# Kernel tuning notes

Hardware: AMD Instinct MI355X
Metric: run time of the kernel (lower is better)

## Reference

```python
import jax, jax.numpy as jnp
import numpy as np

D_MODEL = 1024
N_HEADS = 16
HEAD_DIM = D_MODEL // N_HEADS


def setup_inputs() -> dict:
    key = jax.random.key(0)
    ks = jax.random.split(key, 11)
    B, S = 4, 2048
    scale = 1.0 / np.sqrt(D_MODEL)
    inp = {
        "Q": jax.random.normal(ks[0], (B, S, D_MODEL), jnp.float32),
        "K": jax.random.normal(ks[1], (B, S, D_MODEL), jnp.float32),
        "V": jax.random.normal(ks[2], (B, S, D_MODEL), jnp.float32),
        "Wq": jax.random.normal(ks[3], (D_MODEL, D_MODEL), jnp.float32) * scale,
        "bq": jnp.zeros((D_MODEL,), jnp.float32),
        "Wk": jax.random.normal(ks[4], (D_MODEL, D_MODEL), jnp.float32) * scale,
        "bk": jnp.zeros((D_MODEL,), jnp.float32),
        "Wv": jax.random.normal(ks[5], (D_MODEL, D_MODEL), jnp.float32) * scale,
        "bv": jnp.zeros((D_MODEL,), jnp.float32),
        "Wo": jax.random.normal(ks[6], (D_MODEL, D_MODEL), jnp.float32) * scale,
        "bo": jnp.zeros((D_MODEL,), jnp.float32),
    }
    return inp


def reference(Q, K, V, Wq, bq, Wk, bk, Wv, bv, Wo, bo):
    B, S, _ = Q.shape
    # Linear projections (torch nn.Linear: x @ W.T + b)
    q = Q @ Wq.T + bq
    k = K @ Wk.T + bk
    v = V @ Wv.T + bv
    # [B, S, H, Dh] -> [B, H, S, Dh]
    q = q.reshape(B, S, N_HEADS, HEAD_DIM).transpose(0, 2, 1, 3)
    k = k.reshape(B, S, N_HEADS, HEAD_DIM).transpose(0, 2, 1, 3)
    v = v.reshape(B, S, N_HEADS, HEAD_DIM).transpose(0, 2, 1, 3)
    inv_sqrt_dh = 1.0 / np.sqrt(HEAD_DIM)
    scores = jnp.einsum("bhqd,bhkd->bhqk", q, k) * inv_sqrt_dh  # [B,H,S,S]
    attn = jax.nn.softmax(scores, axis=-1)
    out = jnp.einsum("bhqk,bhkd->bhqd", attn, v)  # [B,H,S,Dh]
    out = out.transpose(0, 2, 1, 3).reshape(B, S, D_MODEL)
    return out @ Wo.T + bo
```

## Files before the change

### kernel.cpp

```cpp
#include <hip/hip_runtime.h>
#include <hip/hip_bf16.h>
#include <stdint.h>
#include <stddef.h>


typedef __bf16 bf16_t;
typedef __bf16 bf16x4 __attribute__((ext_vector_type(4)));
typedef __bf16 bf16x8 __attribute__((ext_vector_type(8)));
typedef float f32x4 __attribute__((ext_vector_type(4)));

#define D_MODEL 1024
#define M_ROWS  8192
#define S_LEN   2048
#define N_HEADS 16
#define HEAD_DIM 64
#define GBK 32
#define NT (D_MODEL / GBK)

__device__ __forceinline__ void async_copy16(void* lds, const void* g) {
    __builtin_amdgcn_global_load_lds(
        (const __attribute__((address_space(1))) void*)g,
        (__attribute__((address_space(3))) void*)lds, 16, 0, 0);
}

__device__ __forceinline__ uint32_t cvt_pk_bf16(float lo, float hi) {
    uint32_t r;
    asm("v_cvt_pk_bf16_f32 %0, %1, %2" : "=v"(r) : "v"(lo), "v"(hi));
    return r;
}

__global__ __launch_bounds__(256) void conv_w(
    const float* __restrict__ s0, const float* __restrict__ s1, const float* __restrict__ s2,
    bf16_t* __restrict__ d0, bf16_t* __restrict__ d1, bf16_t* __restrict__ d2)
{
    const float* s; bf16_t* d;
    if (blockIdx.y == 0)      { s = s0; d = d0; }
    else if (blockIdx.y == 1) { s = s1; d = d1; }
    else                      { s = s2; d = d2; }
    const int i = (blockIdx.x * 256 + threadIdx.x) * 8;
    const f32x4 a = *(const f32x4*)(s + i);
    const f32x4 b = *(const f32x4*)(s + i + 4);
    bf16x8 o;
#pragma unroll
    for (int j = 0; j < 4; j++) { o[j] = (bf16_t)a[j]; o[4 + j] = (bf16_t)b[j]; }
    *(bf16x8*)(d + i) = o;
}

__global__ __launch_bounds__(256, 3) void gemm_proj(
    const float* __restrict__ A0, const bf16_t* __restrict__ W0, const float* __restrict__ b0,
    const float* __restrict__ A1, const bf16_t* __restrict__ W1, const float* __restrict__ b1,
    const float* __restrict__ A2, const bf16_t* __restrict__ W2, const float* __restrict__ b2,
    bf16_t* C0, bf16_t* C1, bf16_t* C2)
{
    const int lin = blockIdx.x + ((int)blockIdx.y << 3) + ((int)blockIdx.z << 9);
    const int nl  = (lin & 7) * 192 + (lin >> 3);
    const int z   = nl >> 9;
    const int rem = nl & 511;
    const int bm0 = (rem >> 3) * 128;
    const int bn0 = (rem & 7) * 128;

    const float* A; const bf16_t* W; const float* bias; bf16_t* C;
    if (z == 0)      { A = A0; W = W0; bias = b0; C = C0; }
    else if (z == 1) { A = A1; W = W1; bias = b1; C = C1; }
    else             { A = A2; W = W2; bias = b2; C = C2; }
    const float cs = (z == 0) ? 0.125f : (z == 1) ? 1.4426950408889634f : 1.0f;

    __align__(16) __shared__ bf16_t sA[2][128 * 36];
    __align__(16) __shared__ bf16_t sW[2][128 * GBK];

    const int t    = threadIdx.x;
    const int lane = t & 63;
    const int w    = t >> 6;
    const int wm   = (w & 1) * 64;
    const int wn   = (w >> 1) * 64;
    const int q4   = lane >> 4;
    const int l16  = lane & 15;

    const int srow  = t >> 1;
    const int cbase = (t & 1) * 2;
    const float* aptr = &A[(size_t)(bm0 + srow) * D_MODEL + cbase * 8];

    auto stageW = [&](int buf, int kt) {
#pragma unroll
        for (int i = 0; i < 2; i++) {
            const int cid = i * 256 + t;
            const int row = cid >> 2;
            const int cg  = (cid & 3) ^ (row & 3);
            async_copy16(&sW[buf][cid * 8],
                         &W[(size_t)(bn0 + row) * D_MODEL + kt * GBK + cg * 8]);
        }
    };

    f32x4 arA[4], arB[4];
#pragma unroll
    for (int c = 0; c < 4; c++) {
        arA[c] = *(const f32x4*)(aptr + c * 4);
        arB[c] = *(const f32x4*)(aptr + GBK + c * 4);
    }
    stageW(0, 0);

    f32x4 acc[4][4];
    const f32x4 zero4 = {0.f, 0.f, 0.f, 0.f};
#pragma unroll
    for (int i = 0; i < 4; i++)
#pragma unroll
        for (int j = 0; j < 4; j++) acc[i][j] = zero4;

    auto body = [&](int kt, int buf, f32x4 (&ar)[4]) {
        bf16x8 abf[2];
#pragma unroll
        for (int c = 0; c < 4; c++)
#pragma unroll
            for (int j = 0; j < 4; j++)
                abf[c >> 1][(c & 1) * 4 + j] = (bf16_t)ar[c][j];
#pragma unroll
        for (int hb = 0; hb < 2; hb++) {
            const int slot = (cbase + hb) ^ (srow & 3);
            *(bf16x8*)&sA[buf][srow * 36 + slot * 8] = abf[hb];
        }
        __syncthreads();
        if (kt + 2 < NT) {
            const float* ap = aptr + (size_t)(kt + 2) * GBK;
#pragma unroll
            for (int c = 0; c < 4; c++) ar[c] = *(const f32x4*)(ap + c * 4);
        }
        if (kt + 1 < NT) stageW(buf ^ 1, kt + 1);

        bf16x8 af[4], bfr[4];
#pragma unroll
        for (int i = 0; i < 4; i++) {
            const int m = wm + i * 16 + l16;
            af[i]  = *(const bf16x8*)&sA[buf][m * 36 + (q4 ^ (m & 3)) * 8];
            const int n = wn + i * 16 + l16;
            bfr[i] = *(const bf16x8*)&sW[buf][n * GBK + (q4 ^ (n & 3)) * 8];
        }
#pragma unroll
        for (int i = 0; i < 4; i++)
#pragma unroll
            for (int j = 0; j < 4; j++)
                acc[i][j] = __builtin_amdgcn_mfma_f32_16x16x32_bf16(af[i], bfr[j], acc[i][j], 0, 0, 0);
    };

    for (int kt = 0; kt < NT; kt += 2) {
        body(kt,     0, arA);
        body(kt + 1, 1, arB);
    }

    if (z != 2) {
#pragma unroll
        for (int j = 0; j < 4; j++) {
            const int col = bn0 + wn + j * 16 + l16;
            const float bj = bias[col];
#pragma unroll
            for (int i = 0; i < 4; i++) {
                const int rowb = bm0 + wm + i * 16 + q4 * 4;
#pragma unroll
                for (int r = 0; r < 4; r++)
                    C[(size_t)(rowb + r) * D_MODEL + col] = (bf16_t)((acc[i][j][r] + bj) * cs);
            }
        }
    } else {
        const int bb = bm0 >> 11;
        const int sbase = (bm0 & 2047) + wm;
#pragma unroll
        for (int j = 0; j < 4; j++) {
            const int col = bn0 + wn + j * 16 + l16;
            const float bj = bias[col];
            bf16_t* ct = C + ((size_t)bb * 1024 + col) * 2048;
#pragma unroll
            for (int i = 0; i < 4; i++) {
                const int s0 = sbase + i * 16 + q4 * 4;
                const int s0p = (s0 & ~31) | (((s0 >> 2) & 3) << 3) | (((s0 >> 4) & 1) << 2);
                bf16x4 v4;
#pragma unroll
                for (int r = 0; r < 4; r++) v4[r] = (bf16_t)(acc[i][j][r] + bj);
                *(bf16x4*)&ct[s0p] = v4;
            }
        }
    }
}

__global__ __launch_bounds__(256, 3) void gemm_out(
    const bf16_t* __restrict__ A, const bf16_t* __restrict__ W,
    const float* __restrict__ bias, float* __restrict__ C)
{
    const int lin = blockIdx.x + ((int)blockIdx.y << 3);
    const int nl  = (lin & 7) * 64 + (lin >> 3);
    const int bm0 = (nl >> 3) * 128;
    const int bn0 = (nl & 7) * 128;

    __align__(16) __shared__ bf16_t sA[2][128 * GBK];
    __align__(16) __shared__ bf16_t sW[2][128 * GBK];

    const int t    = threadIdx.x;
    const int lane = t & 63;
    const int w    = t >> 6;
    const int wm   = (w & 1) * 64;
    const int wn   = (w >> 1) * 64;
    const int q4   = lane >> 4;
    const int l16  = lane & 15;

    auto stage = [&](int buf, int kt) {
#pragma unroll
        for (int i = 0; i < 2; i++) {
            const int cid = i * 256 + t;
            const int row = cid >> 2;
            const int cg  = (cid & 3) ^ (row & 3);
            async_copy16(&sA[buf][cid * 8],
                         &A[(size_t)(bm0 + row) * D_MODEL + kt * GBK + cg * 8]);
            async_copy16(&sW[buf][cid * 8],
                         &W[(size_t)(bn0 + row) * D_MODEL + kt * GBK + cg * 8]);
        }
    };

    stage(0, 0);

    f32x4 acc[4][4];
    const f32x4 zero4 = {0.f, 0.f, 0.f, 0.f};
#pragma unroll
    for (int i = 0; i < 4; i++)
#pragma unroll
        for (int j = 0; j < 4; j++) acc[i][j] = zero4;

    for (int kt = 0; kt < NT; ++kt) {
        const int buf = kt & 1;
        __syncthreads();
        if (kt + 1 < NT) stage(buf ^ 1, kt + 1);

        bf16x8 af[4], bfr[4];
#pragma unroll
        for (int i = 0; i < 4; i++) {
            const int m = wm + i * 16 + l16;
            af[i]  = *(const bf16x8*)&sA[buf][m * GBK + (q4 ^ (m & 3)) * 8];
            const int n = wn + i * 16 + l16;
            bfr[i] = *(const bf16x8*)&sW[buf][n * GBK + (q4 ^ (n & 3)) * 8];
        }
#pragma unroll
        for (int i = 0; i < 4; i++)
#pragma unroll
            for (int j = 0; j < 4; j++)
                acc[i][j] = __builtin_amdgcn_mfma_f32_16x16x32_bf16(af[i], bfr[j], acc[i][j], 0, 0, 0);
    }

#pragma unroll
    for (int j = 0; j < 4; j++) {
        const int col = bn0 + wn + j * 16 + l16;
        const float bj = bias[col];
#pragma unroll
        for (int i = 0; i < 4; i++) {
            const int rowb = bm0 + wm + i * 16 + q4 * 4;
#pragma unroll
            for (int r = 0; r < 4; r++)
                C[(size_t)(rowb + r) * D_MODEL + col] = acc[i][j][r] + bj;
        }
    }
}

#define KVT (S_LEN / 128)

__global__ __launch_bounds__(512, 3) void attn_fused(
    const bf16_t* __restrict__ q, const bf16_t* __restrict__ k,
    const bf16_t* __restrict__ vt, bf16_t* o)
{
    __align__(16) __shared__ bf16_t sK[2][128 * 64];
    __align__(16) __shared__ bf16_t sVt[2][64 * 128];

    const int t    = threadIdx.x;
    const int lane = t & 63;
    const int w    = t >> 6;
    const int head = blockIdx.x;
    const int b    = head >> 4;
    const int h    = head & 15;
    const size_t base = (size_t)b * S_LEN * D_MODEL + (size_t)h * HEAD_DIM;
    const bf16_t* vth = vt + ((size_t)b * 1024 + h * 64) * 2048;
    const int qt0  = blockIdx.y * 256;
    const int q4   = lane >> 4;
    const int l16  = lane & 15;

    bf16x8 qf[2][2];
#pragma unroll
    for (int mg = 0; mg < 2; mg++)
#pragma unroll
        for (int kk = 0; kk < 2; kk++)
            qf[mg][kk] = *(const bf16x8*)&q[base + (size_t)(qt0 + w * 32 + mg * 16 + l16) * D_MODEL + kk * 32 + q4 * 8];

    const f32x4 zero4 = {0.f, 0.f, 0.f, 0.f};
    f32x4 oacc[2][4];
#pragma unroll
    for (int mg = 0; mg < 2; mg++)
#pragma unroll
        for (int g = 0; g < 4; g++) oacc[mg][g] = zero4;
    f32x4 sacc[2] = {zero4, zero4};

    bf16x8 ones;
#pragma unroll
    for (int j = 0; j < 8; j++) ones[j] = (bf16_t)1.0f;

    auto stage = [&](int bf, int kt) {
        const int key0 = kt * 128;
#pragma unroll
        for (int i = 0; i < 2; i++) {
            const int cid = i * 512 + t;
            const int row = cid >> 3;
            const int cg  = (cid & 7) ^ (row & 7);
            async_copy16(&sK[bf][cid * 8], &k[base + (size_t)(key0 + row) * D_MODEL + cg * 8]);
        }
#pragma unroll
        for (int i = 0; i < 2; i++) {
            const int cid = i * 512 + t;
            const int dh  = cid >> 4;
            const int cg  = (cid & 15) ^ (dh & 15);
            async_copy16(&sVt[bf][cid * 8], &vth[(size_t)dh * 2048 + key0 + cg * 8]);
        }
    };

    stage(0, 0);
    asm volatile("s_waitcnt vmcnt(0)" ::: "memory");
    __builtin_amdgcn_s_barrier();
    __builtin_amdgcn_sched_barrier(0);

    for (int kt = 0; kt < KVT; ++kt) {
        const int cur = kt & 1;
        if (kt < KVT - 1) stage(cur ^ 1, kt + 1);

#pragma unroll
        for (int hh = 0; hh < 2; hh++) {
            f32x4 sc[2][4];
            __builtin_amdgcn_s_setprio(1);
#pragma unroll
            for (int ngl = 0; ngl < 4; ngl++) {
                const int key = (hh * 4 + ngl) * 16 + l16;
                const bf16x8 kf0 = *(const bf16x8*)&sK[cur][key * 64 + ((q4) ^ (key & 7)) * 8];
                const bf16x8 kf1 = *(const bf16x8*)&sK[cur][key * 64 + ((4 + q4) ^ (key & 7)) * 8];
#pragma unroll
                for (int mg = 0; mg < 2; mg++) {
                    sc[mg][ngl] = __builtin_amdgcn_mfma_f32_16x16x32_bf16(kf0, qf[mg][0], zero4, 0, 0, 0);
                    sc[mg][ngl] = __builtin_amdgcn_mfma_f32_16x16x32_bf16(kf1, qf[mg][1], sc[mg][ngl], 0, 0, 0);
                }
            }
            __builtin_amdgcn_s_setprio(0);

            bf16x8 pf[2][2];
#pragma unroll
            for (int mg = 0; mg < 2; mg++) {
#pragma unroll
                for (int ngl = 0; ngl < 4; ngl++)
#pragma unroll
                    for (int r = 0; r < 4; r++)
                        sc[mg][ngl][r] = exp2f(sc[mg][ngl][r]);
#pragma unroll
                for (int cl = 0; cl < 2; cl++) {
                    union { uint32_t u[4]; bf16x8 v; } pk;
#pragma unroll
                    for (int dw = 0; dw < 4; dw++) {
                        const int c = cl * 2 + (dw >> 1);
                        const int e = (dw & 1) * 2;
                        pk.u[dw] = cvt_pk_bf16(sc[mg][c][e], sc[mg][c][e + 1]);
                    }
                    pf[mg][cl] = pk.v;
                }
            }

            __builtin_amdgcn_s_setprio(1);
#pragma unroll
            for (int cl = 0; cl < 2; cl++) {
                const int cb = (hh * 2 + cl) * 4;
#pragma unroll
                for (int g = 0; g < 4; g++) {
                    const int dh = g * 16 + l16;
                    const bf16x8 vf = *(const bf16x8*)&sVt[cur][dh * 128 + ((cb + q4) ^ l16) * 8];
#pragma unroll
                    for (int mg = 0; mg < 2; mg++)
                        oacc[mg][g] = __builtin_amdgcn_mfma_f32_16x16x32_bf16(pf[mg][cl], vf, oacc[mg][g], 0, 0, 0);
                }
#pragma unroll
                for (int mg = 0; mg < 2; mg++)
                    sacc[mg] = __builtin_amdgcn_mfma_f32_16x16x32_bf16(pf[mg][cl], ones, sacc[mg], 0, 0, 0);
            }
            __builtin_amdgcn_s_setprio(0);
        }

        asm volatile("s_waitcnt vmcnt(0)" ::: "memory");
        __builtin_amdgcn_s_barrier();
        __builtin_amdgcn_sched_barrier(0);
    }

#pragma unroll
    for (int mg = 0; mg < 2; mg++)
#pragma unroll
        for (int r = 0; r < 4; r++) {
            const float inv = 1.0f / sacc[mg][r];
            const size_t rowoff = base + (size_t)(qt0 + w * 32 + mg * 16 + q4 * 4 + r) * D_MODEL;
#pragma unroll
            for (int g = 0; g < 4; g++)
                o[rowoff + g * 16 + l16] = (bf16_t)(oacc[mg][g][r] * inv);
        }
}

extern "C" void kernel_launch(void* const* d_in, const int* in_sizes, int n_in,
                              void* d_out, int out_size, void* d_ws, size_t ws_size,
                              hipStream_t stream) {
    const float* Q  = (const float*)d_in[0];
    const float* K  = (const float*)d_in[1];
    const float* V  = (const float*)d_in[2];
    const float* Wq = (const float*)d_in[3];
    const float* bq = (const float*)d_in[4];
    const float* Wk = (const float*)d_in[5];
    const float* bk = (const float*)d_in[6];
    const float* Wv = (const float*)d_in[7];
    const float* bv = (const float*)d_in[8];
    const float* Wo = (const float*)d_in[9];
    const float* bo = (const float*)d_in[10];
    float* out = (float*)d_out;

    bf16_t* qb  = (bf16_t*)d_ws;
    bf16_t* vb  = qb + (size_t)M_ROWS * D_MODEL;
    bf16_t* kb  = (bf16_t*)d_out;
    bf16_t* wqb = kb + (size_t)M_ROWS * D_MODEL;
    bf16_t* wkb = wqb + (size_t)D_MODEL * D_MODEL;
    bf16_t* wvb = wkb + (size_t)D_MODEL * D_MODEL;
    bf16_t* wob = vb;
    bf16_t* ob  = qb;

    conv_w<<<dim3(512, 3), dim3(256), 0, stream>>>(Wq, Wk, Wv, wqb, wkb, wvb);
    gemm_proj<<<dim3(8, 64, 3), dim3(256), 0, stream>>>(Q, wqb, bq, K, wkb, bk, V, wvb, bv, qb, kb, vb);
    attn_fused<<<dim3(4 * N_HEADS, S_LEN / 256), dim3(512), 0, stream>>>(qb, kb, vb, ob);
    conv_w<<<dim3(512, 1), dim3(256), 0, stream>>>(Wo, Wo, Wo, wob, wob, wob);
    gemm_out<<<dim3(8, 64), dim3(256), 0, stream>>>(ob, wob, bo, out);
}
```

Baseline: 375.9 us.

## Pipeline projection GEMM with one barrier per tile and adjust LDS swizzle

Result: faster. 358.3 us (-4.7%).

```diff
diff --git a/kernel.cpp b/kernel.cpp
--- a/kernel.cpp
+++ b/kernel.cpp
@@ -85,28 +85,12 @@
         for (int i = 0; i < 2; i++) {
             const int cid = i * 256 + t;
             const int row = cid >> 2;
-            const int cg  = (cid & 3) ^ (row & 3);
+            const int cg  = (cid & 3) ^ ((row >> 1) & 3);
             async_copy16(&sW[buf][cid * 8],
                          &W[(size_t)(bn0 + row) * D_MODEL + kt * GBK + cg * 8]);
         }
     };
-
-    f32x4 arA[4], arB[4];
-#pragma unroll
-    for (int c = 0; c < 4; c++) {
-        arA[c] = *(const f32x4*)(aptr + c * 4);
-        arB[c] = *(const f32x4*)(aptr + GBK + c * 4);
-    }
-    stageW(0, 0);
-
-    f32x4 acc[4][4];
-    const f32x4 zero4 = {0.f, 0.f, 0.f, 0.f};
-#pragma unroll
-    for (int i = 0; i < 4; i++)
-#pragma unroll
-        for (int j = 0; j < 4; j++) acc[i][j] = zero4;
-
-    auto body = [&](int kt, int buf, f32x4 (&ar)[4]) {
+    auto writeA = [&](int buf, f32x4 (&ar)[4]) {
         bf16x8 abf[2];
 #pragma unroll
         for (int c = 0; c < 4; c++)
@@ -118,13 +102,33 @@
             const int slot = (cbase + hb) ^ (srow & 3);
             *(bf16x8*)&sA[buf][srow * 36 + slot * 8] = abf[hb];
         }
-        __syncthreads();
+    };
+
+    stageW(0, 0);
+    f32x4 arA[4], arB[4];
+#pragma unroll
+    for (int c = 0; c < 4; c++) arA[c] = *(const f32x4*)(aptr + c * 4);
+#pragma unroll
+    for (int c = 0; c < 4; c++) arB[c] = *(const f32x4*)(aptr + GBK + c * 4);
+    writeA(0, arA);
+    asm volatile("s_waitcnt vmcnt(4) lgkmcnt(0)" ::: "memory");
+    __builtin_amdgcn_s_barrier();
+    __builtin_amdgcn_sched_barrier(0);
+
+    f32x4 acc[4][4];
+    const f32x4 zero4 = {0.f, 0.f, 0.f, 0.f};
+#pragma unroll
+    for (int i = 0; i < 4; i++)
+#pragma unroll
+        for (int j = 0; j < 4; j++) acc[i][j] = zero4;
+
+    auto body = [&](int kt, int buf, f32x4 (&arCur)[4], f32x4 (&arNext)[4]) {
+        if (kt + 1 < NT) stageW(buf ^ 1, kt + 1);
         if (kt + 2 < NT) {
             const float* ap = aptr + (size_t)(kt + 2) * GBK;
 #pragma unroll
-            for (int c = 0; c < 4; c++) ar[c] = *(const f32x4*)(ap + c * 4);
-        }
-        if (kt + 1 < NT) stageW(buf ^ 1, kt + 1);
+            for (int c = 0; c < 4; c++) arNext[c] = *(const f32x4*)(ap + c * 4);
+        }
 
         bf16x8 af[4], bfr[4];
 #pragma unroll
@@ -132,18 +136,25 @@
             const int m = wm + i * 16 + l16;
             af[i]  = *(const bf16x8*)&sA[buf][m * 36 + (q4 ^ (m & 3)) * 8];
             const int n = wn + i * 16 + l16;
-            bfr[i] = *(const bf16x8*)&sW[buf][n * GBK + (q4 ^ (n & 3)) * 8];
+            bfr[i] = *(const bf16x8*)&sW[buf][n * GBK + (q4 ^ ((n >> 1) & 3)) * 8];
         }
 #pragma unroll
         for (int i = 0; i < 4; i++)
 #pragma unroll
             for (int j = 0; j < 4; j++)
                 acc[i][j] = __builtin_amdgcn_mfma_f32_16x16x32_bf16(af[i], bfr[j], acc[i][j], 0, 0, 0);
+
+        __builtin_amdgcn_sched_barrier(0);
+        if (kt + 1 < NT) writeA(buf ^ 1, arCur);
+        if (kt + 2 < NT) asm volatile("s_waitcnt vmcnt(4) lgkmcnt(0)" ::: "memory");
+        else             asm volatile("s_waitcnt vmcnt(0) lgkmcnt(0)" ::: "memory");
+        __builtin_amdgcn_s_barrier();
+        __builtin_amdgcn_sched_barrier(0);
     };
 
     for (int kt = 0; kt < NT; kt += 2) {
-        body(kt,     0, arA);
-        body(kt + 1, 1, arB);
+        body(kt,     0, arB, arA);
+        body(kt + 1, 1, arA, arB);
     }
 
     if (z != 2) {
@@ -205,7 +216,7 @@
         for (int i = 0; i < 2; i++) {
             const int cid = i * 256 + t;
             const int row = cid >> 2;
-            const int cg  = (cid & 3) ^ (row & 3);
+            const int cg  = (cid & 3) ^ ((row >> 1) & 3);
             async_copy16(&sA[buf][cid * 8],
                          &A[(size_t)(bm0 + row) * D_MODEL + kt * GBK + cg * 8]);
             async_copy16(&sW[buf][cid * 8],
@@ -231,9 +242,9 @@
 #pragma unroll
         for (int i = 0; i < 4; i++) {
             const int m = wm + i * 16 + l16;
-            af[i]  = *(const bf16x8*)&sA[buf][m * GBK + (q4 ^ (m & 3)) * 8];
+            af[i]  = *(const bf16x8*)&sA[buf][m * GBK + (q4 ^ ((m >> 1) & 3)) * 8];
             const int n = wn + i * 16 + l16;
-            bfr[i] = *(const bf16x8*)&sW[buf][n * GBK + (q4 ^ (n & 3)) * 8];
+            bfr[i] = *(const bf16x8*)&sW[buf][n * GBK + (q4 ^ ((n >> 1) & 3)) * 8];
         }
 #pragma unroll
         for (int i = 0; i < 4; i++)
```
